# Optimization experiments

Measured on AMD Instinct MI355X. Metric: run time of the kernel, lower is better.

Reference implementation:

```python
import jax, jax.numpy as jnp
import numpy as np

EPS = 1e-10
BETA_SCALE = 1.0
TEMP = 0.5


def setup_inputs() -> dict:
    key = jax.random.key(0)
    ks = jax.random.split(key, 8)
    D = 128
    return {
        "root_mu_min": jax.random.normal(ks[0], (1, 64, D), dtype=jnp.float32),
        "root_mu_max": jax.random.normal(ks[1], (1, 64, D), dtype=jnp.float32),
        "root_beta_min_raw": jax.random.normal(ks[2], (1, 64, D), dtype=jnp.float32),
        "root_beta_max_raw": jax.random.normal(ks[3], (1, 64, D), dtype=jnp.float32),
        "adj_logits0": jax.random.normal(ks[4], (512, 64), dtype=jnp.float32),
        "adj_logits1": jax.random.normal(ks[5], (2048, 512), dtype=jnp.float32),
        "u0": jax.random.uniform(ks[6], (1, 512, 64), dtype=jnp.float32),
        "u1": jax.random.uniform(ks[7], (1, 2048, 512), dtype=jnp.float32),
    }


def _gumbel_sigmoid_hard(logits, u):
    # gumbel noise from externally supplied uniforms, straight-through hard threshold
    g = -jnp.log(-jnp.log(u + EPS) + EPS)
    y_soft = jax.nn.sigmoid((logits + g) / TEMP)
    y_hard = (y_soft > 0.5).astype(y_soft.dtype)
    return y_hard - jax.lax.stop_gradient(y_soft) + y_soft


def _weighted_intersection(mu_min, mu_max, beta_min, beta_max, w):
    # w: (1, C, P); parent boxes: (1, P, D)
    wsum = jnp.sum(w, axis=2)[..., None] + EPS                      # (1, C, 1)
    b_min = jnp.einsum('bcp,bpd->bcd', w, beta_min) / wsum           # (1, C, D)
    b_max = jnp.einsum('bcp,bpd->bcd', w, beta_max) / wsum           # (1, C, D)
    logw = jnp.log(w + EPS)[..., None]                               # (1, C, P, 1)
    arg_min = logw + mu_min[:, None, :, :] / b_min[:, :, None, :]    # (1, C, P, D)
    mu_min_i = b_min * jax.nn.logsumexp(arg_min, axis=2)             # (1, C, D)
    arg_max = logw - mu_max[:, None, :, :] / b_max[:, :, None, :]    # (1, C, P, D)
    mu_max_i = -b_max * jax.nn.logsumexp(arg_max, axis=2)            # (1, C, D)
    return mu_min_i, mu_max_i, b_min, b_max


def reference(root_mu_min, root_mu_max, root_beta_min_raw, root_beta_max_raw,
              adj_logits0, adj_logits1, u0, u1):
    beta_min = jax.nn.sigmoid(root_beta_min_raw) * BETA_SCALE + 1e-6
    beta_max = jax.nn.sigmoid(root_beta_max_raw) * BETA_SCALE + 1e-6
    level = (root_mu_min, root_mu_max, beta_min, beta_max)
    outs = list(level)
    for logits, u in ((adj_logits0, u0), (adj_logits1, u1)):
        w = _gumbel_sigmoid_hard(logits[None], u)  # (1, C, P)
        level = _weighted_intersection(*level, w)
        outs.extend(level)
    return tuple(outs)
```

## Files before the change

### kernel.cpp

```cpp
#include <hip/hip_runtime.h>
#include <cmath>

#define DD 128
#define LOG2E 1.4426950408889634f
#define MMARGIN 4.16f

__device__ __forceinline__ float sigm(float x) { return 1.0f / (1.0f + __expf(-x)); }

__global__ __launch_bounds__(512, 4)
void k_lvl1(const float* __restrict__ mu_min0, const float* __restrict__ mu_max0,
            const float* __restrict__ braw_min, const float* __restrict__ braw_max,
            const float* __restrict__ adj0, const float* __restrict__ u0,
            float* __restrict__ out,
            float2* __restrict__ mu2_1, float2* __restrict__ bb2_1,
            float4* __restrict__ pmaxf) {
    __shared__ float wsh[64];
    __shared__ int npres;
    __shared__ float4 red[8][64];
    __shared__ float4 cmx[8][64];
    __shared__ float4 carrA[64], carrB[64];
    const int tid = threadIdx.x;
    const int w = tid >> 6, lane = tid & 63;
    const int c = blockIdx.x;

    if (tid < 16) {
        int i = blockIdx.x * 16 + tid;
        out[i] = mu_min0[i];
        out[8192 + i] = mu_max0[i];
        out[16384 + i] = sigm(braw_min[i]) + 1e-6f;
        out[24576 + i] = sigm(braw_max[i]) + 1e-6f;
    }

    if (tid < 64) {
        int idx = c * 64 + tid;
        float uu = u0[idx] + 1e-10f;
        float g = -__logf(-__logf(uu) + 1e-10f);
        bool pres = (adj0[idx] + g) > 0.0f;
        wsh[tid] = pres ? 1.0f : 1e-10f;
        unsigned long long m = __ballot(pres);
        if (tid == 0) npres = (int)__popcll(m);
    }
    __syncthreads();

    const int p0 = w * 8;
    const int dbase = 2 * lane;

    float4 accB = make_float4(0.f, 0.f, 0.f, 0.f);
    float4 mrow[8];
    float wreg[8];
    float cm_mn0 = -INFINITY, cm_mn1 = -INFINITY, cm_ng0 = -INFINITY, cm_ng1 = -INFINITY;
    #pragma unroll
    for (int z = 0; z < 8; ++z) {
        int p = p0 + z;
        float2 bmr = *(const float2*)(braw_min + p * DD + dbase);
        float2 bxr = *(const float2*)(braw_max + p * DD + dbase);
        float2 mnr = *(const float2*)(mu_min0 + p * DD + dbase);
        float2 mxr = *(const float2*)(mu_max0 + p * DD + dbase);
        float bm0 = sigm(bmr.x) + 1e-6f, bm1 = sigm(bmr.y) + 1e-6f;
        float bx0 = sigm(bxr.x) + 1e-6f, bx1 = sigm(bxr.y) + 1e-6f;
        mrow[z] = make_float4(mnr.x, mxr.x, mnr.y, mxr.y);
        cm_mn0 = fmaxf(cm_mn0, mnr.x); cm_mn1 = fmaxf(cm_mn1, mnr.y);
        cm_ng0 = fmaxf(cm_ng0, -mxr.x); cm_ng1 = fmaxf(cm_ng1, -mxr.y);
        float wv = wsh[p];
        wreg[z] = wv;
        accB.x = fmaf(wv, bm0, accB.x);
        accB.y = fmaf(wv, bx0, accB.y);
        accB.z = fmaf(wv, bm1, accB.z);
        accB.w = fmaf(wv, bx1, accB.w);
    }
    red[w][lane] = accB;
    cmx[w][lane] = make_float4(cm_mn0, cm_ng0, cm_mn1, cm_ng1);
    __syncthreads();

    float bmin0, bmax0, bmin1, bmax1, rmin0, rmin1, nrmax0, nrmax1, Mm0, Mm1, Mg0, Mg1;
    if (tid < 64) {
        float4 S = red[0][lane];
        float4 M = cmx[0][lane];
        #pragma unroll
        for (int ww = 1; ww < 8; ++ww) {
            float4 t = red[ww][lane];
            S.x += t.x; S.y += t.y; S.z += t.z; S.w += t.w;
            float4 m = cmx[ww][lane];
            M.x = fmaxf(M.x, m.x); M.y = fmaxf(M.y, m.y);
            M.z = fmaxf(M.z, m.z); M.w = fmaxf(M.w, m.w);
        }
        Mm0 = M.x; Mg0 = M.y; Mm1 = M.z; Mg1 = M.w;
        if (c == 0) {
            pmaxf[lane] = make_float4(Mm0 + MMARGIN, Mg0 + MMARGIN,
                                      Mm1 + MMARGIN, Mg1 + MMARGIN);
        }
        const float wsv = (float)npres + 1e-10f;
        bmin0 = S.x / wsv; bmax0 = S.y / wsv; bmin1 = S.z / wsv; bmax1 = S.w / wsv;
        rmin0 = 1.0f / fmaxf(bmin0, 1e-30f);
        rmin1 = 1.0f / fmaxf(bmin1, 1e-30f);
        nrmax0 = -1.0f / fmaxf(bmax0, 1e-30f);
        nrmax1 = -1.0f / fmaxf(bmax1, 1e-30f);
        float rm20 = rmin0 * LOG2E, rm21 = rmin1 * LOG2E;
        float nx20 = nrmax0 * LOG2E, nx21 = nrmax1 * LOG2E;
        carrA[lane] = make_float4(rm20, rm21, nx20, nx21);
        carrB[lane] = make_float4(-rm20 * Mm0, -rm21 * Mm1, nx20 * Mg0, nx21 * Mg1);
    }
    __syncthreads();

    float4 cA = carrA[lane], cB = carrB[lane];

    float4 accS = make_float4(0.f, 0.f, 0.f, 0.f);
    #pragma unroll
    for (int z = 0; z < 8; ++z) {
        float4 q = mrow[z];
        float wv = wreg[z];
        accS.x = fmaf(wv, __builtin_amdgcn_exp2f(fmaf(q.x, cA.x, cB.x)), accS.x);
        accS.y = fmaf(wv, __builtin_amdgcn_exp2f(fmaf(q.y, cA.z, cB.z)), accS.y);
        accS.z = fmaf(wv, __builtin_amdgcn_exp2f(fmaf(q.z, cA.y, cB.y)), accS.z);
        accS.w = fmaf(wv, __builtin_amdgcn_exp2f(fmaf(q.w, cA.w, cB.w)), accS.w);
    }
    red[w][lane] = accS;
    __syncthreads();

    if (tid < 64) {
        float4 S = red[0][lane];
        #pragma unroll
        for (int ww = 1; ww < 8; ++ww) {
            float4 t = red[ww][lane];
            S.x += t.x; S.y += t.y; S.z += t.z; S.w += t.w;
        }
        const float S10 = fmaxf(S.x, 1e-35f);
        const float S20 = fmaxf(S.y, 1e-35f);
        const float S11 = fmaxf(S.z, 1e-35f);
        const float S21 = fmaxf(S.w, 1e-35f);
        const int idx = c * DD + 2 * lane;
        float v10 = bmin0 * fmaf(rmin0, Mm0, __logf(S10));
        float v11 = bmin1 * fmaf(rmin1, Mm1, __logf(S11));
        float v20 = -bmax0 * fmaf(-nrmax0, Mg0, __logf(S20));
        float v21 = -bmax1 * fmaf(-nrmax1, Mg1, __logf(S21));
        *(float2*)(out + 32768 + idx)  = make_float2(v10, v11);
        *(float2*)(out + 98304 + idx)  = make_float2(v20, v21);
        *(float2*)(out + 163840 + idx) = make_float2(bmin0, bmin1);
        *(float2*)(out + 229376 + idx) = make_float2(bmax0, bmax1);
        *(float4*)(mu2_1 + idx) = make_float4(v10, v20, v11, v21);
        *(float4*)(bb2_1 + idx) = make_float4(bmin0, bmax0, bmin1, bmax1);
    }
}

__global__ __launch_bounds__(512, 4)
void k_level2d(const float* __restrict__ logits, const float* __restrict__ u,
               const float2* __restrict__ bb2, const float2* __restrict__ mu2,
               const float4* __restrict__ pmaxf,
               float* __restrict__ o_mu_min, float* __restrict__ o_mu_max,
               float* __restrict__ o_b_min, float* __restrict__ o_b_max) {
    constexpr int P = 512, TC = 4;
    __shared__ __align__(16) float wsh[P][TC];
    __shared__ int npres[TC];
    __shared__ float4 red[8][TC][64];
    __shared__ float4 carrA[TC][64], carrB[TC][64];
    const int tid = threadIdx.x;
    const int w = tid >> 6;
    const int lane = tid & 63;
    const int c0 = blockIdx.x * TC;
    if (tid < TC) npres[tid] = 0;
    __syncthreads();

    #pragma unroll
    for (int it = 0; it < TC; ++it) {
        int idx = (c0 + it) * P + tid;
        float uu = u[idx] + 1e-10f;
        float g = -__logf(-__logf(uu) + 1e-10f);
        bool pres = (logits[idx] + g) > 0.0f;
        wsh[tid][it] = pres ? 1.0f : 1e-10f;
        unsigned long long m = __ballot(pres);
        if (lane == 0) atomicAdd(&npres[it], (int)__popcll(m));
    }
    __syncthreads();

    const unsigned lb = (unsigned)(lane << 4);
    const char* bbc = (const char*)bb2 + (unsigned)(w * 64) * 1024u + lb;
    const char* muc = (const char*)mu2 + (unsigned)(w * 64) * 1024u + lb;
    const int p0 = w * 64;

    float4 accB[TC];
    #pragma unroll
    for (int j = 0; j < TC; ++j) accB[j] = make_float4(0.f, 0.f, 0.f, 0.f);
    for (int z = 0; z < 64; z += 4) {
        float4 q0 = *(const float4*)(bbc + (unsigned)(z + 0) * 1024u);
        float4 q1 = *(const float4*)(bbc + (unsigned)(z + 1) * 1024u);
        float4 q2 = *(const float4*)(bbc + (unsigned)(z + 2) * 1024u);
        float4 q3 = *(const float4*)(bbc + (unsigned)(z + 3) * 1024u);
        float4 w0 = *(const float4*)wsh[p0 + z + 0];
        float4 w1 = *(const float4*)wsh[p0 + z + 1];
        float4 w2 = *(const float4*)wsh[p0 + z + 2];
        float4 w3 = *(const float4*)wsh[p0 + z + 3];
        const float* wf0 = (const float*)&w0;
        const float* wf1 = (const float*)&w1;
        const float* wf2 = (const float*)&w2;
        const float* wf3 = (const float*)&w3;
        #pragma unroll
        for (int j = 0; j < TC; ++j) {
            accB[j].x = fmaf(wf0[j], q0.x, accB[j].x);
            accB[j].y = fmaf(wf0[j], q0.y, accB[j].y);
            accB[j].z = fmaf(wf0[j], q0.z, accB[j].z);
            accB[j].w = fmaf(wf0[j], q0.w, accB[j].w);
        }
        #pragma unroll
        for (int j = 0; j < TC; ++j) {
            accB[j].x = fmaf(wf1[j], q1.x, accB[j].x);
            accB[j].y = fmaf(wf1[j], q1.y, accB[j].y);
            accB[j].z = fmaf(wf1[j], q1.z, accB[j].z);
            accB[j].w = fmaf(wf1[j], q1.w, accB[j].w);
        }
        #pragma unroll
        for (int j = 0; j < TC; ++j) {
            accB[j].x = fmaf(wf2[j], q2.x, accB[j].x);
            accB[j].y = fmaf(wf2[j], q2.y, accB[j].y);
            accB[j].z = fmaf(wf2[j], q2.z, accB[j].z);
            accB[j].w = fmaf(wf2[j], q2.w, accB[j].w);
        }
        #pragma unroll
        for (int j = 0; j < TC; ++j) {
            accB[j].x = fmaf(wf3[j], q3.x, accB[j].x);
            accB[j].y = fmaf(wf3[j], q3.y, accB[j].y);
            accB[j].z = fmaf(wf3[j], q3.z, accB[j].z);
            accB[j].w = fmaf(wf3[j], q3.w, accB[j].w);
        }
    }
    #pragma unroll
    for (int j = 0; j < TC; ++j) red[w][j][lane] = accB[j];
    __syncthreads();

    float bmin0, bmax0, bmin1, bmax1, rmin0, rmin1, nrmax0, nrmax1, Mm0, Mm1, Mg0, Mg1;
    const int rj = tid >> 6;
    if (tid < 256) {
        float4 S = red[0][rj][lane];
        #pragma unroll
        for (int ww = 1; ww < 8; ++ww) {
            float4 t = red[ww][rj][lane];
            S.x += t.x; S.y += t.y; S.z += t.z; S.w += t.w;
        }
        float4 km = pmaxf[lane];
        Mm0 = km.x; Mg0 = km.y; Mm1 = km.z; Mg1 = km.w;
        const float wsv = (float)npres[rj] + 1e-10f;
        bmin0 = S.x / wsv; bmax0 = S.y / wsv; bmin1 = S.z / wsv; bmax1 = S.w / wsv;
        rmin0 = 1.0f / fmaxf(bmin0, 1e-30f);
        rmin1 = 1.0f / fmaxf(bmin1, 1e-30f);
        nrmax0 = -1.0f / fmaxf(bmax0, 1e-30f);
        nrmax1 = -1.0f / fmaxf(bmax1, 1e-30f);
        float rm20 = rmin0 * LOG2E, rm21 = rmin1 * LOG2E;
        float nx20 = nrmax0 * LOG2E, nx21 = nrmax1 * LOG2E;
        carrA[rj][lane] = make_float4(rm20, rm21, nx20, nx21);
        carrB[rj][lane] = make_float4(-rm20 * Mm0, -rm21 * Mm1, nx20 * Mg0, nx21 * Mg1);
    }
    __syncthreads();

    float4 cA[TC], cB[TC];
    #pragma unroll
    for (int j = 0; j < TC; ++j) { cA[j] = carrA[j][lane]; cB[j] = carrB[j][lane]; }

    float4 accS[TC];
    #pragma unroll
    for (int j = 0; j < TC; ++j) accS[j] = make_float4(0.f, 0.f, 0.f, 0.f);
    for (int z = 0; z < 64; z += 4) {
        float4 q0 = *(const float4*)(muc + (unsigned)(z + 0) * 1024u);
        float4 q1 = *(const float4*)(muc + (unsigned)(z + 1) * 1024u);
        float4 q2 = *(const float4*)(muc + (unsigned)(z + 2) * 1024u);
        float4 q3 = *(const float4*)(muc + (unsigned)(z + 3) * 1024u);
        float4 w0 = *(const float4*)wsh[p0 + z + 0];
        float4 w1 = *(const float4*)wsh[p0 + z + 1];
        float4 w2 = *(const float4*)wsh[p0 + z + 2];
        float4 w3 = *(const float4*)wsh[p0 + z + 3];
        const float* wf0 = (const float*)&w0;
        const float* wf1 = (const float*)&w1;
        const float* wf2 = (const float*)&w2;
        const float* wf3 = (const float*)&w3;
        #pragma unroll
        for (int j = 0; j < TC; ++j) {
            if (wf0[j] > 0.5f) {
                accS[j].x += __builtin_amdgcn_exp2f(fmaf(q0.x, cA[j].x, cB[j].x));
                accS[j].y += __builtin_amdgcn_exp2f(fmaf(q0.y, cA[j].z, cB[j].z));
                accS[j].z += __builtin_amdgcn_exp2f(fmaf(q0.z, cA[j].y, cB[j].y));
                accS[j].w += __builtin_amdgcn_exp2f(fmaf(q0.w, cA[j].w, cB[j].w));
            }
            if (wf1[j] > 0.5f) {
                accS[j].x += __builtin_amdgcn_exp2f(fmaf(q1.x, cA[j].x, cB[j].x));
                accS[j].y += __builtin_amdgcn_exp2f(fmaf(q1.y, cA[j].z, cB[j].z));
                accS[j].z += __builtin_amdgcn_exp2f(fmaf(q1.z, cA[j].y, cB[j].y));
                accS[j].w += __builtin_amdgcn_exp2f(fmaf(q1.w, cA[j].w, cB[j].w));
            }
            if (wf2[j] > 0.5f) {
                accS[j].x += __builtin_amdgcn_exp2f(fmaf(q2.x, cA[j].x, cB[j].x));
                accS[j].y += __builtin_amdgcn_exp2f(fmaf(q2.y, cA[j].z, cB[j].z));
                accS[j].z += __builtin_amdgcn_exp2f(fmaf(q2.z, cA[j].y, cB[j].y));
                accS[j].w += __builtin_amdgcn_exp2f(fmaf(q2.w, cA[j].w, cB[j].w));
            }
            if (wf3[j] > 0.5f) {
                accS[j].x += __builtin_amdgcn_exp2f(fmaf(q3.x, cA[j].x, cB[j].x));
                accS[j].y += __builtin_amdgcn_exp2f(fmaf(q3.y, cA[j].z, cB[j].z));
                accS[j].z += __builtin_amdgcn_exp2f(fmaf(q3.z, cA[j].y, cB[j].y));
                accS[j].w += __builtin_amdgcn_exp2f(fmaf(q3.w, cA[j].w, cB[j].w));
            }
        }
    }
    #pragma unroll
    for (int j = 0; j < TC; ++j) red[w][j][lane] = accS[j];
    __syncthreads();

    if (tid < 256) {
        float4 S = red[0][rj][lane];
        #pragma unroll
        for (int ww = 1; ww < 8; ++ww) {
            float4 t = red[ww][rj][lane];
            S.x += t.x; S.y += t.y; S.z += t.z; S.w += t.w;
        }
        const float S10 = fmaxf(S.x, 1e-35f);
        const float S20 = fmaxf(S.y, 1e-35f);
        const float S11 = fmaxf(S.z, 1e-35f);
        const float S21 = fmaxf(S.w, 1e-35f);
        const int idx = (c0 + rj) * DD + 2 * lane;
        float v10 = bmin0 * fmaf(rmin0, Mm0, __logf(S10));
        float v11 = bmin1 * fmaf(rmin1, Mm1, __logf(S11));
        float v20 = -bmax0 * fmaf(-nrmax0, Mg0, __logf(S20));
        float v21 = -bmax1 * fmaf(-nrmax1, Mg1, __logf(S21));
        *(float2*)(o_mu_min + idx) = make_float2(v10, v11);
        *(float2*)(o_mu_max + idx) = make_float2(v20, v21);
        *(float2*)(o_b_min + idx)  = make_float2(bmin0, bmin1);
        *(float2*)(o_b_max + idx)  = make_float2(bmax0, bmax1);
    }
}

extern "C" void kernel_launch(void* const* d_in, const int* in_sizes, int n_in,
                              void* d_out, int out_size, void* d_ws, size_t ws_size,
                              hipStream_t stream) {
    const float* mu_min0  = (const float*)d_in[0];
    const float* mu_max0  = (const float*)d_in[1];
    const float* braw_min = (const float*)d_in[2];
    const float* braw_max = (const float*)d_in[3];
    const float* adj0     = (const float*)d_in[4];
    const float* adj1     = (const float*)d_in[5];
    const float* u0       = (const float*)d_in[6];
    const float* u1       = (const float*)d_in[7];
    float* out = (float*)d_out;
    float* ws = (float*)d_ws;

    float4* pmaxf = (float4*)ws;
    float2* mu2_1 = (float2*)(ws + 256);
    float2* bb2_1 = mu2_1 + 512 * DD;


    k_lvl1<<<dim3(512), dim3(512), 0, stream>>>(
        mu_min0, mu_max0, braw_min, braw_max, adj0, u0,
        out, mu2_1, bb2_1, pmaxf);

    k_level2d<<<dim3(512), dim3(512), 0, stream>>>(
        adj1, u1, bb2_1, mu2_1, pmaxf,
        out + 294912, out + 557056, out + 819200, out + 1081344);
}
```

Measured before the change: 113.8 us.

## Stage parent box loads into LDS via async global_load_lds ring buffer

In the level-2 kernel, both parent-data loops no longer read global memory straight into registers. Each warp now streams rows into a private 4-slot LDS ring with async global-to-LDS loads, prefetching two rows ahead and gating reads with explicit vmcnt/lgkmcnt waits. The reduction scratch buffer is reused as this staging area. The goal is to overlap global load latency with the FMA and exp2 work, at the cost of extra LDS traffic, hand-placed wait instructions and scheduling barriers that limit compiler reordering.

```diff
diff --git a/kernel.cpp b/kernel.cpp
--- a/kernel.cpp
+++ b/kernel.cpp
@@ -6,6 +6,11 @@
 #define MMARGIN 4.16f
 
 __device__ __forceinline__ float sigm(float x) { return 1.0f / (1.0f + __expf(-x)); }
+
+#define STAGE(GP, LP)                                                     \
+    __builtin_amdgcn_global_load_lds(                                     \
+        (__attribute__((address_space(1))) void*)(GP),                    \
+        (__attribute__((address_space(3))) void*)(LP), 16, 0, 0)
 
 __global__ __launch_bounds__(512, 4)
 void k_lvl1(const float* __restrict__ mu_min0, const float* __restrict__ mu_max0,
@@ -151,8 +156,9 @@
     constexpr int P = 512, TC = 4;
     __shared__ __align__(16) float wsh[P][TC];
     __shared__ int npres[TC];
-    __shared__ float4 red[8][TC][64];
+    __shared__ __align__(16) char redarena[32768];
     __shared__ float4 carrA[TC][64], carrB[TC][64];
+    float4 (*red)[TC][64] = (float4(*)[TC][64])redarena;
     const int tid = threadIdx.x;
     const int w = tid >> 6;
     const int lane = tid & 63;
@@ -176,23 +182,26 @@
     const char* bbc = (const char*)bb2 + (unsigned)(w * 64) * 1024u + lb;
     const char* muc = (const char*)mu2 + (unsigned)(w * 64) * 1024u + lb;
     const int p0 = w * 64;
+    char* arena = redarena + (w << 12);
 
     float4 accB[TC];
     #pragma unroll
     for (int j = 0; j < TC; ++j) accB[j] = make_float4(0.f, 0.f, 0.f, 0.f);
-    for (int z = 0; z < 64; z += 4) {
-        float4 q0 = *(const float4*)(bbc + (unsigned)(z + 0) * 1024u);
-        float4 q1 = *(const float4*)(bbc + (unsigned)(z + 1) * 1024u);
-        float4 q2 = *(const float4*)(bbc + (unsigned)(z + 2) * 1024u);
-        float4 q3 = *(const float4*)(bbc + (unsigned)(z + 3) * 1024u);
+
+    STAGE(bbc + 0u,    arena);
+    STAGE(bbc + 1024u, arena + 1024);
+    STAGE(bbc + 2048u, arena + 2048);
+    STAGE(bbc + 3072u, arena + 3072);
+    for (int z = 0; z < 64; z += 2) {
+        if (z < 62) { asm volatile("s_waitcnt vmcnt(2)" ::: "memory"); }
+        else        { asm volatile("s_waitcnt vmcnt(0)" ::: "memory"); }
+        __builtin_amdgcn_sched_barrier(0);
+        float4 q0 = *(const float4*)(arena + ((z & 3) << 10) + lb);
+        float4 q1 = *(const float4*)(arena + (((z + 1) & 3) << 10) + lb);
         float4 w0 = *(const float4*)wsh[p0 + z + 0];
         float4 w1 = *(const float4*)wsh[p0 + z + 1];
-        float4 w2 = *(const float4*)wsh[p0 + z + 2];
-        float4 w3 = *(const float4*)wsh[p0 + z + 3];
         const float* wf0 = (const float*)&w0;
         const float* wf1 = (const float*)&w1;
-        const float* wf2 = (const float*)&w2;
-        const float* wf3 = (const float*)&w3;
         #pragma unroll
         for (int j = 0; j < TC; ++j) {
             accB[j].x = fmaf(wf0[j], q0.x, accB[j].x);
@@ -207,19 +216,11 @@
             accB[j].z = fmaf(wf1[j], q1.z, accB[j].z);
             accB[j].w = fmaf(wf1[j], q1.w, accB[j].w);
         }
-        #pragma unroll
-        for (int j = 0; j < TC; ++j) {
-            accB[j].x = fmaf(wf2[j], q2.x, accB[j].x);
-            accB[j].y = fmaf(wf2[j], q2.y, accB[j].y);
-            accB[j].z = fmaf(wf2[j], q2.z, accB[j].z);
-            accB[j].w = fmaf(wf2[j], q2.w, accB[j].w);
-        }
-        #pragma unroll
-        for (int j = 0; j < TC; ++j) {
-            accB[j].x = fmaf(wf3[j], q3.x, accB[j].x);
-            accB[j].y = fmaf(wf3[j], q3.y, accB[j].y);
-            accB[j].z = fmaf(wf3[j], q3.z, accB[j].z);
-            accB[j].w = fmaf(wf3[j], q3.w, accB[j].w);
+        asm volatile("s_waitcnt lgkmcnt(0)" ::: "memory");
+        __builtin_amdgcn_sched_barrier(0);
+        if (z + 4 < 64) {
+            STAGE(bbc + (unsigned)(z + 4) * 1024u, arena + ((z & 3) << 10));
+            STAGE(bbc + (unsigned)(z + 5) * 1024u, arena + (((z + 1) & 3) << 10));
         }
     }
     #pragma unroll
@@ -257,19 +258,21 @@
     float4 accS[TC];
     #pragma unroll
     for (int j = 0; j < TC; ++j) accS[j] = make_float4(0.f, 0.f, 0.f, 0.f);
-    for (int z = 0; z < 64; z += 4) {
-        float4 q0 = *(const float4*)(muc + (unsigned)(z + 0) * 1024u);
-        float4 q1 = *(const float4*)(muc + (unsigned)(z + 1) * 1024u);
-        float4 q2 = *(const float4*)(muc + (unsigned)(z + 2) * 1024u);
-        float4 q3 = *(const float4*)(muc + (unsigned)(z + 3) * 1024u);
+
+    STAGE(muc + 0u,    arena);
+    STAGE(muc + 1024u, arena + 1024);
+    STAGE(muc + 2048u, arena + 2048);
+    STAGE(muc + 3072u, arena + 3072);
+    for (int z = 0; z < 64; z += 2) {
+        if (z < 62) { asm volatile("s_waitcnt vmcnt(2)" ::: "memory"); }
+        else        { asm volatile("s_waitcnt vmcnt(0)" ::: "memory"); }
+        __builtin_amdgcn_sched_barrier(0);
+        float4 q0 = *(const float4*)(arena + ((z & 3) << 10) + lb);
+        float4 q1 = *(const float4*)(arena + (((z + 1) & 3) << 10) + lb);
         float4 w0 = *(const float4*)wsh[p0 + z + 0];
         float4 w1 = *(const float4*)wsh[p0 + z + 1];
-        float4 w2 = *(const float4*)wsh[p0 + z + 2];
-        float4 w3 = *(const float4*)wsh[p0 + z + 3];
         const float* wf0 = (const float*)&w0;
         const float* wf1 = (const float*)&w1;
-        const float* wf2 = (const float*)&w2;
-        const float* wf3 = (const float*)&w3;
         #pragma unroll
         for (int j = 0; j < TC; ++j) {
             if (wf0[j] > 0.5f) {
@@ -284,18 +287,12 @@
                 accS[j].z += __builtin_amdgcn_exp2f(fmaf(q1.z, cA[j].y, cB[j].y));
                 accS[j].w += __builtin_amdgcn_exp2f(fmaf(q1.w, cA[j].w, cB[j].w));
             }
-            if (wf2[j] > 0.5f) {
-                accS[j].x += __builtin_amdgcn_exp2f(fmaf(q2.x, cA[j].x, cB[j].x));
-                accS[j].y += __builtin_amdgcn_exp2f(fmaf(q2.y, cA[j].z, cB[j].z));
-                accS[j].z += __builtin_amdgcn_exp2f(fmaf(q2.z, cA[j].y, cB[j].y));
-                accS[j].w += __builtin_amdgcn_exp2f(fmaf(q2.w, cA[j].w, cB[j].w));
-            }
-            if (wf3[j] > 0.5f) {
-                accS[j].x += __builtin_amdgcn_exp2f(fmaf(q3.x, cA[j].x, cB[j].x));
-                accS[j].y += __builtin_amdgcn_exp2f(fmaf(q3.y, cA[j].z, cB[j].z));
-                accS[j].z += __builtin_amdgcn_exp2f(fmaf(q3.z, cA[j].y, cB[j].y));
-                accS[j].w += __builtin_amdgcn_exp2f(fmaf(q3.w, cA[j].w, cB[j].w));
-            }
+        }
+        asm volatile("s_waitcnt lgkmcnt(0)" ::: "memory");
+        __builtin_amdgcn_sched_barrier(0);
+        if (z + 4 < 64) {
+            STAGE(muc + (unsigned)(z + 4) * 1024u, arena + ((z & 3) << 10));
+            STAGE(muc + (unsigned)(z + 5) * 1024u, arena + (((z + 1) & 3) << 10));
         }
     }
     #pragma unroll
```

Result: slower. 118.9 us (+4.5%).
